# Kernel optimization log

Hardware: AMD Instinct MI355X
Metric: run time of the kernel (lower is better)

Reference implementation:

```python
import jax, jax.numpy as jnp
import numpy as np
import math

D_MODEL = 1024
EPS = 1e-6  # RMSNorm epsilon


def setup_inputs() -> dict:
    key = jax.random.key(0)
    ks = jax.random.split(key, 9)
    d = D_MODEL
    B, T = 4, 4096
    s = 1.0 / math.sqrt(d)
    return {
        "x": jax.random.normal(ks[0], (B, T, d), dtype=jnp.float32),
        "w_key": jax.random.normal(ks[1], (2 * d, d), dtype=jnp.float32) * s,  # Linear(d, 2d, bias=False)
        "conv_w": jax.random.normal(ks[2], (d, 1, 3), dtype=jnp.float32) * (1.0 / math.sqrt(3)),  # depthwise k=3
        "conv_b": jax.random.normal(ks[3], (d,), dtype=jnp.float32) * 0.02,
        "w1": jax.random.normal(ks[4], (2 * d, d), dtype=jnp.float32) * s,  # Linear(d, 2d)
        "b1": jax.random.normal(ks[5], (2 * d,), dtype=jnp.float32) * 0.02,
        "w2": jax.random.normal(ks[6], (d, 2 * d), dtype=jnp.float32) * (1.0 / math.sqrt(2 * d)),  # Linear(2d, d)
        "b2": jax.random.normal(ks[7], (d,), dtype=jnp.float32) * 0.02,
        "norm_w": jnp.ones((d,), dtype=jnp.float32),
    }


def parallel_lerp_scan(theta, alpha):
    # h_t = lerp(h_{t-1}, theta_t, alpha_t) = (1-alpha_t)*h_{t-1} + alpha_t*theta_t
    # Linear recurrence h_t = a_t*h_{t-1} + b_t -> log-depth associative scan.
    a = 1.0 - alpha
    b = alpha * theta

    def combine(c1, c2):
        a1, b1 = c1
        a2, b2 = c2
        return (a2 * a1, a2 * b1 + b2)

    _, h = jax.lax.associative_scan(combine, (a, b), axis=1)
    return h


def rms_norm(x, w):
    var = jnp.mean(jnp.square(x), axis=-1, keepdims=True)
    return x * jax.lax.rsqrt(var + EPS) * w


def reference(x, w_key, conv_w, conv_b, w1, b1, w2, b2, norm_w):
    d = x.shape[-1]
    res = jnp.einsum('btd,ed->bte', x, w_key)  # [B,T,2D]
    theta, alpha = res[..., :d], res[..., d:]
    h = parallel_lerp_scan(jnp.tanh(theta) * math.pi, jax.nn.sigmoid(alpha))
    h = h.astype(x.dtype)
    # causal depthwise conv: left-pad (k-1)=2 zeros along time
    h_t = jnp.transpose(h, (0, 2, 1))  # [B,D,T]
    conv = jax.lax.conv_general_dilated(
        h_t, conv_w, window_strides=(1,), padding=[(2, 0)],
        feature_group_count=d, dimension_numbers=('NCH', 'OIH', 'NCH'))
    h_bound = jnp.transpose(conv + conv_b[None, :, None], (0, 2, 1))  # [B,T,D]
    z = h + h_bound
    hid = jax.nn.silu(jnp.einsum('btd,ed->bte', z, w1) + b1)
    h_final = jnp.einsum('bte,de->btd', hid, w2) + b2
    return rms_norm(h_final, norm_w)
```

## Files before the change

kernel.cpp:

```cpp
#include <hip/hip_runtime.h>

typedef unsigned short u16;
typedef unsigned int u32;
typedef __attribute__((ext_vector_type(8))) short short8;
typedef __attribute__((ext_vector_type(4))) float f32x4;

#define T_LEN 4096
#define BATCH 4
#define M_TOT (BATCH*T_LEN)
#define NCHUNK 32
#define CLEN 128

__device__ __forceinline__ u16 f2bf(float f){
  u32 u = __builtin_bit_cast(u32, f);
  u32 r = (u + 0x7FFFu + ((u >> 16) & 1u)) >> 16;
  return (u16)r;
}
__device__ __forceinline__ float sigmoid_(float v){ return 1.f/(1.f + __expf(-v)); }
__device__ __forceinline__ float tanh_pi_(float v){
  return 3.14159265358979323846f * (1.f - 2.f/(1.f + __expf(2.f*v)));
}

__global__ __launch_bounds__(256) void cvt_bf16_k(const float* __restrict__ in,
                                                  u16* __restrict__ out, int n4){
  int g = blockIdx.x*256 + threadIdx.x;
  if (g >= n4) return;
  float4 v = reinterpret_cast<const float4*>(in)[g];
  reinterpret_cast<ushort4*>(out)[g] =
      make_ushort4(f2bf(v.x), f2bf(v.y), f2bf(v.z), f2bf(v.w));
}


#define BAR() __builtin_amdgcn_s_barrier()
#define WAITLGKM0() asm volatile("s_waitcnt lgkmcnt(0)" ::: "memory")
#define VMCNT(n) asm volatile("s_waitcnt vmcnt(" #n ")" ::: "memory")

#define STAGE(buf, ab, q, kt) do { \
  const u16* _s = ((ab) ? Bb : Ab) + (size_t)(q)*rowK64 + (size_t)(kt)*64; \
  __builtin_amdgcn_global_load_lds( \
    (const __attribute__((address_space(1))) void*)_s, \
    (__attribute__((address_space(3))) void*)(smem + (buf)*65536 + (ab)*32768 + (q)*8192 + stb), \
    16, 0, 0); \
} while(0)

#define LDA(buf, m, kk) (*(const short8*)(smem + (buf)*65536 + aRow + (m)*2048 + ((kk) ? csw1 : csw0)))
#define LDB(buf, n, kk) (*(const short8*)(smem + (buf)*65536 + 32768 + bRow + (n)*2048 + ((kk) ? csw1 : csw0)))

#define LOADB(buf) do { _Pragma("unroll") for (int n=0;n<4;n++){ \
    bfr0[n] = LDB(buf,n,0); bfr1[n] = LDB(buf,n,1); } } while(0)

#define PHASE_Q(buf, q, STMTS, ENDSTMT) do { \
  short8 _a00 = LDA(buf, 2*(q)  , 0); \
  short8 _a01 = LDA(buf, 2*(q)  , 1); \
  short8 _a10 = LDA(buf, 2*(q)+1, 0); \
  short8 _a11 = LDA(buf, 2*(q)+1, 1); \
  STMTS \
  BAR(); \
  WAITLGKM0(); \
  __builtin_amdgcn_s_setprio(1); \
  _Pragma("unroll") \
  for (int n=0;n<4;n++){ \
    acc[2*(q)][n]   = __builtin_amdgcn_mfma_f32_16x16x32_bf16(_a00, bfr0[n], acc[2*(q)][n], 0,0,0); \
    acc[2*(q)][n]   = __builtin_amdgcn_mfma_f32_16x16x32_bf16(_a01, bfr1[n], acc[2*(q)][n], 0,0,0); \
    acc[2*(q)+1][n] = __builtin_amdgcn_mfma_f32_16x16x32_bf16(_a10, bfr0[n], acc[2*(q)+1][n], 0,0,0); \
    acc[2*(q)+1][n] = __builtin_amdgcn_mfma_f32_16x16x32_bf16(_a11, bfr1[n], acc[2*(q)+1][n], 0,0,0); \
  } \
  __builtin_amdgcn_s_setprio(0); \
  ENDSTMT \
  BAR(); \
} while(0)

template<int EPI>
__global__ __launch_bounds__(512, 2) void gemm8p(
    const u16* __restrict__ Ag, const u16* __restrict__ Bg,
    const float* __restrict__ bias, void* __restrict__ Cout,
    int M, int N, int K)
{
  extern __shared__ __attribute__((aligned(16))) char smem[];
  const int tid = threadIdx.x;
  const int wid = tid >> 6, lane = tid & 63;
  const int wr = wid >> 2, wc = wid & 3;
  const int fr = lane & 15, fq = lane >> 4;

  const int nbn = N >> 8;
  const int nwg = gridDim.x;
  const int bid = blockIdx.x;
  const int swzb = (bid & 7) * (nwg >> 3) + (bid >> 3);
  const int bm = swzb / nbn, bn = swzb - bm * nbn;

  const size_t rowK64 = (size_t)64 * K;
  const u16* Ab = Ag + ((size_t)bm*256 + (tid>>3)) * K + ((tid & 7) ^ ((tid >> 3) & 7)) * 8;
  const u16* Bb = Bg + ((size_t)bn*256 + (tid>>3)) * K + ((tid & 7) ^ ((tid >> 3) & 7)) * 8;
  const u32 stb = (u32)(wid << 10);

  const u32 aRow = (u32)(wr*128 + fr) * 128;
  const u32 bRow = (u32)(wc*64  + fr) * 128;
  const u32 csw0 = (u32)((fq*16)      ^ ((fr & 7) << 4));
  const u32 csw1 = (u32)((64 + fq*16) ^ ((fr & 7) << 4));

  f32x4 acc[8][4];
#pragma unroll
  for (int m=0;m<8;m++)
#pragma unroll
    for (int n=0;n<4;n++) acc[m][n] = f32x4{0.f,0.f,0.f,0.f};

  short8 bfr0[4], bfr1[4];

  const int NT = K >> 6;

  STAGE(0,1,0,0); STAGE(0,1,1,0); STAGE(0,1,2,0); STAGE(0,1,3,0);
  STAGE(0,0,0,0); STAGE(0,0,1,0); STAGE(0,0,2,0); STAGE(0,0,3,0);
  STAGE(1,1,0,1); STAGE(1,1,1,1); STAGE(1,1,2,1); STAGE(1,1,3,1);
  STAGE(1,0,0,1); STAGE(1,0,2,1);
  VMCNT(6);
  BAR();

  for (int i = 0; i < (NT>>1) - 1; ++i){
    const int tt = 2*i;
    PHASE_Q(0, 0, LOADB(0); STAGE(1,0,1,tt+1); STAGE(1,0,3,tt+1);, );
    PHASE_Q(0, 1, STAGE(0,1,0,tt+2); STAGE(0,1,1,tt+2);, );
    PHASE_Q(0, 2, STAGE(0,1,2,tt+2); STAGE(0,1,3,tt+2);, );
    PHASE_Q(0, 3, STAGE(0,0,0,tt+2); STAGE(0,0,2,tt+2);, VMCNT(6); );
    PHASE_Q(1, 0, LOADB(1); STAGE(0,0,1,tt+2); STAGE(0,0,3,tt+2);, );
    PHASE_Q(1, 1, STAGE(1,1,0,tt+3); STAGE(1,1,1,tt+3);, );
    PHASE_Q(1, 2, STAGE(1,1,2,tt+3); STAGE(1,1,3,tt+3);, );
    PHASE_Q(1, 3, STAGE(1,0,0,tt+3); STAGE(1,0,2,tt+3);, VMCNT(6); );
  }
  {
    const int tt = NT-2;
    PHASE_Q(0, 0, LOADB(0); STAGE(1,0,1,tt+1); STAGE(1,0,3,tt+1);, );
    PHASE_Q(0, 1, , );
    PHASE_Q(0, 2, , );
    PHASE_Q(0, 3, , VMCNT(0); );
    PHASE_Q(1, 0, LOADB(1);, );
    PHASE_Q(1, 1, , );
    PHASE_Q(1, 2, , );
    PHASE_Q(1, 3, , );
  }

  const int orow0 = bm*256 + wr*128;
  const int ocol0 = bn*256 + wc*64;
#pragma unroll
  for (int m=0;m<8;m++){
#pragma unroll
    for (int n=0;n<4;n++){
      const int col = ocol0 + n*16 + fr;
#pragma unroll
      for (int r=0;r<4;r++){
        const int row = orow0 + m*16 + fq*4 + r;
        float v = acc[m][n][r];
        if constexpr (EPI == 0){
          float o = (col < 1024) ? tanh_pi_(v) : sigmoid_(v);
          ((float*)Cout)[(size_t)row*N + col] = o;
        } else if constexpr (EPI == 1){
          v += bias[col];
          ((u16*)Cout)[(size_t)row*N + col] = f2bf(v * sigmoid_(v));
        } else {
          v += bias[col];
          ((float*)Cout)[(size_t)row*N + col] = v;
        }
      }
    }
  }
}

__global__ __launch_bounds__(256) void scan_stage1(const float* __restrict__ res,
                                                   float* __restrict__ sA,
                                                   float* __restrict__ sB,
                                                   float* __restrict__ sA2,
                                                   float* __restrict__ sB2){
  const int c     = (blockIdx.x & 3)*256 + threadIdx.x;
  const int chunk = (blockIdx.x >> 2) & (NCHUNK-1);
  const int b     = blockIdx.x >> 7;
  const float* p = res + ((size_t)(b*T_LEN + chunk*CLEN))*2048 + c;
  float A = 1.f, Bv = 0.f;
#pragma unroll 4
  for (int t=0;t<CLEN-1;++t){
    float th = p[0];
    float s  = p[1024];
    float a  = 1.f - s;
    A  *= a;
    Bv  = a*Bv + s*th;
    p  += 2048;
  }
  const int idx = (b*NCHUNK + chunk)*1024 + c;
  sA2[idx] = A; sB2[idx] = Bv;
  {
    float th = p[0];
    float s  = p[1024];
    float a  = 1.f - s;
    A  *= a;
    Bv  = a*Bv + s*th;
  }
  sA[idx] = A; sB[idx] = Bv;
}

__global__ __launch_bounds__(256) void scan_stage2(const float* __restrict__ sA,
                                                   const float* __restrict__ sB,
                                                   float* __restrict__ Hp){
  const int g = blockIdx.x*256 + threadIdx.x;
  const int b = g >> 10, c = g & 1023;
  float H = 0.f;
#pragma unroll
  for (int i=0;i<NCHUNK;++i){
    const int idx = (b*NCHUNK + i)*1024 + c;
    Hp[idx] = H;
    H = sA[idx]*H + sB[idx];
  }
}

__global__ __launch_bounds__(256) void scan3_conv_k(const float* __restrict__ res,
                                                    const float* __restrict__ Hp,
                                                    const float* __restrict__ sA2,
                                                    const float* __restrict__ sB2,
                                                    const float* __restrict__ cw,
                                                    const float* __restrict__ cb,
                                                    u16* __restrict__ z){
  const int c     = (blockIdx.x & 3)*256 + threadIdx.x;
  const int chunk = (blockIdx.x >> 2) & (NCHUNK-1);
  const int b     = blockIdx.x >> 7;
  const float* p = res + ((size_t)(b*T_LEN + chunk*CLEN))*2048 + c;
  u16*         q = z   + ((size_t)(b*T_LEN + chunk*CLEN))*1024 + c;
  const int idx = (b*NCHUNK + chunk)*1024 + c;
  float H   = Hp[idx];
  float hm1 = H;
  float hm2 = 0.f;
  if (chunk > 0){
    const int pidx = idx - 1024;
    hm2 = sA2[pidx]*Hp[pidx] + sB2[pidx];
  }
  const float w0 = cw[3*c], w1 = cw[3*c+1], w2 = cw[3*c+2], bb = cb[c];
#pragma unroll 4
  for (int t=0;t<CLEN;++t){
    float th = p[0];
    float s  = p[1024];
    H = (1.f - s)*H + s*th;
    float v = H + bb + hm2*w0 + hm1*w1 + H*w2;
    q[0] = f2bf(v);
    hm2 = hm1; hm1 = H;
    p += 2048; q += 1024;
  }
}

__global__ __launch_bounds__(256) void rmsnorm_k(float* __restrict__ io,
                                                 const float* __restrict__ w){
  const int row = blockIdx.x;
  const int tid = threadIdx.x;
  float* p = io + (size_t)row*1024;
  float4 v = reinterpret_cast<const float4*>(p)[tid];
  float ss = v.x*v.x + v.y*v.y + v.z*v.z + v.w*v.w;
#pragma unroll
  for (int o=32; o>0; o>>=1) ss += __shfl_xor(ss, o, 64);
  __shared__ float red[4];
  if ((tid & 63) == 0) red[tid >> 6] = ss;
  __syncthreads();
  float tot = red[0] + red[1] + red[2] + red[3];
  float scale = rsqrtf(tot * (1.f/1024.f) + 1e-6f);
  float4 wv = reinterpret_cast<const float4*>(w)[tid];
  float4 o;
  o.x = v.x*scale*wv.x; o.y = v.y*scale*wv.y;
  o.z = v.z*scale*wv.z; o.w = v.w*scale*wv.w;
  reinterpret_cast<float4*>(p)[tid] = o;
}

extern "C" void kernel_launch(void* const* d_in, const int* in_sizes, int n_in,
                              void* d_out, int out_size, void* d_ws, size_t ws_size,
                              hipStream_t stream) {
  const float* x      = (const float*)d_in[0];
  const float* w_key  = (const float*)d_in[1];
  const float* conv_w = (const float*)d_in[2];
  const float* conv_b = (const float*)d_in[3];
  const float* w1     = (const float*)d_in[4];
  const float* b1     = (const float*)d_in[5];
  const float* w2     = (const float*)d_in[6];
  const float* b2     = (const float*)d_in[7];
  const float* norm_w = (const float*)d_in[8];
  float* out = (float*)d_out;
  char*  ws  = (char*)d_ws;

  size_t off = 0;
  float* RES  = (float*)(ws + off); off += (size_t)M_TOT*2048*4;
  u16*   XB   = (u16*)  (ws + off); off += (size_t)M_TOT*1024*2;
  u16*   WK   = (u16*)  (ws + off); off += (size_t)2048*1024*2;
  u16*   W1B  = (u16*)  (ws + off); off += (size_t)2048*1024*2;
  u16*   W2B  = (u16*)  (ws + off); off += (size_t)1024*2048*2;
  float* SA   = (float*)(ws + off); off += (size_t)BATCH*NCHUNK*1024*4;
  float* SB   = (float*)(ws + off); off += (size_t)BATCH*NCHUNK*1024*4;
  float* SA2  = (float*)(ws + off); off += (size_t)BATCH*NCHUNK*1024*4;
  float* SB2  = (float*)(ws + off); off += (size_t)BATCH*NCHUNK*1024*4;
  float* HP   = (float*)(ws + off); off += (size_t)BATCH*NCHUNK*1024*4;
  u16* ZB  = XB;
  u16* HID = (u16*)RES;

  hipFuncSetAttribute((const void*)gemm8p<0>, hipFuncAttributeMaxDynamicSharedMemorySize, 131072);
  hipFuncSetAttribute((const void*)gemm8p<1>, hipFuncAttributeMaxDynamicSharedMemorySize, 131072);
  hipFuncSetAttribute((const void*)gemm8p<2>, hipFuncAttributeMaxDynamicSharedMemorySize, 131072);

  cvt_bf16_k<<<(M_TOT*1024/4 + 255)/256, 256, 0, stream>>>(x,     XB,  M_TOT*1024/4);
  cvt_bf16_k<<<(2048*1024/4  + 255)/256, 256, 0, stream>>>(w_key, WK,  2048*1024/4);
  cvt_bf16_k<<<(2048*1024/4  + 255)/256, 256, 0, stream>>>(w1,    W1B, 2048*1024/4);
  cvt_bf16_k<<<(1024*2048/4  + 255)/256, 256, 0, stream>>>(w2,    W2B, 1024*2048/4);

  gemm8p<0><<<(M_TOT/256)*(2048/256), 512, 131072, stream>>>(XB, WK, nullptr, RES, M_TOT, 2048, 1024);

  scan_stage1<<<BATCH*NCHUNK*4, 256, 0, stream>>>(RES, SA, SB, SA2, SB2);
  scan_stage2<<<16, 256, 0, stream>>>(SA, SB, HP);
  scan3_conv_k<<<BATCH*NCHUNK*4, 256, 0, stream>>>(RES, HP, SA2, SB2, conv_w, conv_b, ZB);

  gemm8p<1><<<(M_TOT/256)*(2048/256), 512, 131072, stream>>>(ZB, W1B, b1, HID, M_TOT, 2048, 1024);

  gemm8p<2><<<(M_TOT/256)*(1024/256), 512, 131072, stream>>>(HID, W2B, b2, out, M_TOT, 1024, 2048);

  rmsnorm_k<<<M_TOT, 256, 0, stream>>>(out, norm_w);
}
```

Before: 328.8 us.

## Software-pipeline LDS fragment loads in GEMM and store scan input as bf16

The GEMM main loop now double-buffers A and B register fragments, issuing the LDS reads for the next quarter-phase during the current MFMA block so LDS latency is hidden behind compute. Separately, the first GEMM's activated theta/alpha output is written as bf16 instead of fp32, halving traffic for that write and for the two scan kernels that read it. The register double-buffering raises VGPR pressure, which could cause spills under the two-blocks-per-CU launch bound. Storing scan inputs in bf16 also reduces the precision of the recurrence inputs.

```diff
diff --git a/kernel.cpp b/kernel.cpp
--- a/kernel.cpp
+++ b/kernel.cpp
@@ -15,6 +15,9 @@
   u32 u = __builtin_bit_cast(u32, f);
   u32 r = (u + 0x7FFFu + ((u >> 16) & 1u)) >> 16;
   return (u16)r;
+}
+__device__ __forceinline__ float bf2f(u16 h){
+  u32 u = ((u32)h) << 16; return __builtin_bit_cast(float, u);
 }
 __device__ __forceinline__ float sigmoid_(float v){ return 1.f/(1.f + __expf(-v)); }
 __device__ __forceinline__ float tanh_pi_(float v){
@@ -30,7 +33,6 @@
       make_ushort4(f2bf(v.x), f2bf(v.y), f2bf(v.z), f2bf(v.w));
 }
 
-
 #define BAR() __builtin_amdgcn_s_barrier()
 #define WAITLGKM0() asm volatile("s_waitcnt lgkmcnt(0)" ::: "memory")
 #define VMCNT(n) asm volatile("s_waitcnt vmcnt(" #n ")" ::: "memory")
@@ -46,29 +48,25 @@
 #define LDA(buf, m, kk) (*(const short8*)(smem + (buf)*65536 + aRow + (m)*2048 + ((kk) ? csw1 : csw0)))
 #define LDB(buf, n, kk) (*(const short8*)(smem + (buf)*65536 + 32768 + bRow + (n)*2048 + ((kk) ? csw1 : csw0)))
 
-#define LOADB(buf) do { _Pragma("unroll") for (int n=0;n<4;n++){ \
-    bfr0[n] = LDB(buf,n,0); bfr1[n] = LDB(buf,n,1); } } while(0)
-
-#define PHASE_Q(buf, q, STMTS, ENDSTMT) do { \
-  short8 _a00 = LDA(buf, 2*(q)  , 0); \
-  short8 _a01 = LDA(buf, 2*(q)  , 1); \
-  short8 _a10 = LDA(buf, 2*(q)+1, 0); \
-  short8 _a11 = LDA(buf, 2*(q)+1, 1); \
-  STMTS \
-  BAR(); \
-  WAITLGKM0(); \
-  __builtin_amdgcn_s_setprio(1); \
-  _Pragma("unroll") \
+#define PFA(dst, buf, q) do { \
+  dst[0] = LDA(buf, 2*(q),   0); \
+  dst[1] = LDA(buf, 2*(q),   1); \
+  dst[2] = LDA(buf, 2*(q)+1, 0); \
+  dst[3] = LDA(buf, 2*(q)+1, 1); } while(0)
+
+#define PFB(d0, d1, buf) do { _Pragma("unroll") \
+  for (int n=0;n<4;n++){ d0[n] = LDB(buf,n,0); d1[n] = LDB(buf,n,1); } } while(0)
+
+#define MFMA_Q(q, A, B0, B1) do { _Pragma("unroll") \
   for (int n=0;n<4;n++){ \
-    acc[2*(q)][n]   = __builtin_amdgcn_mfma_f32_16x16x32_bf16(_a00, bfr0[n], acc[2*(q)][n], 0,0,0); \
-    acc[2*(q)][n]   = __builtin_amdgcn_mfma_f32_16x16x32_bf16(_a01, bfr1[n], acc[2*(q)][n], 0,0,0); \
-    acc[2*(q)+1][n] = __builtin_amdgcn_mfma_f32_16x16x32_bf16(_a10, bfr0[n], acc[2*(q)+1][n], 0,0,0); \
-    acc[2*(q)+1][n] = __builtin_amdgcn_mfma_f32_16x16x32_bf16(_a11, bfr1[n], acc[2*(q)+1][n], 0,0,0); \
-  } \
-  __builtin_amdgcn_s_setprio(0); \
-  ENDSTMT \
-  BAR(); \
-} while(0)
+    acc[2*(q)][n]   = __builtin_amdgcn_mfma_f32_16x16x32_bf16(A[0], B0[n], acc[2*(q)][n], 0,0,0); \
+    acc[2*(q)][n]   = __builtin_amdgcn_mfma_f32_16x16x32_bf16(A[1], B1[n], acc[2*(q)][n], 0,0,0); \
+    acc[2*(q)+1][n] = __builtin_amdgcn_mfma_f32_16x16x32_bf16(A[2], B0[n], acc[2*(q)+1][n], 0,0,0); \
+    acc[2*(q)+1][n] = __builtin_amdgcn_mfma_f32_16x16x32_bf16(A[3], B1[n], acc[2*(q)+1][n], 0,0,0); \
+  } } while(0)
+
+#define PRIO1() __builtin_amdgcn_s_setprio(1)
+#define PRIO0() __builtin_amdgcn_s_setprio(0)
 
 template<int EPI>
 __global__ __launch_bounds__(512, 2) void gemm8p(
@@ -104,7 +102,8 @@
 #pragma unroll
     for (int n=0;n<4;n++) acc[m][n] = f32x4{0.f,0.f,0.f,0.f};
 
-  short8 bfr0[4], bfr1[4];
+  short8 bP0[4], bP1[4], bN0[4], bN1[4];
+  short8 aP[4], aN[4];
 
   const int NT = K >> 6;
 
@@ -114,28 +113,69 @@
   STAGE(1,0,0,1); STAGE(1,0,2,1);
   VMCNT(6);
   BAR();
+  PFB(bP0, bP1, 0);
+  PFA(aP, 0, 0);
 
   for (int i = 0; i < (NT>>1) - 1; ++i){
     const int tt = 2*i;
-    PHASE_Q(0, 0, LOADB(0); STAGE(1,0,1,tt+1); STAGE(1,0,3,tt+1);, );
-    PHASE_Q(0, 1, STAGE(0,1,0,tt+2); STAGE(0,1,1,tt+2);, );
-    PHASE_Q(0, 2, STAGE(0,1,2,tt+2); STAGE(0,1,3,tt+2);, );
-    PHASE_Q(0, 3, STAGE(0,0,0,tt+2); STAGE(0,0,2,tt+2);, VMCNT(6); );
-    PHASE_Q(1, 0, LOADB(1); STAGE(0,0,1,tt+2); STAGE(0,0,3,tt+2);, );
-    PHASE_Q(1, 1, STAGE(1,1,0,tt+3); STAGE(1,1,1,tt+3);, );
-    PHASE_Q(1, 2, STAGE(1,1,2,tt+3); STAGE(1,1,3,tt+3);, );
-    PHASE_Q(1, 3, STAGE(1,0,0,tt+3); STAGE(1,0,2,tt+3);, VMCNT(6); );
+    STAGE(1,0,1,tt+1); STAGE(1,0,3,tt+1);
+    BAR(); WAITLGKM0();
+    PRIO1(); MFMA_Q(0, aP, bP0, bP1); PFA(aN, 0, 1); PRIO0();
+    BAR();
+    STAGE(0,1,0,tt+2); STAGE(0,1,1,tt+2);
+    BAR(); WAITLGKM0();
+    PRIO1(); MFMA_Q(1, aN, bP0, bP1); PFA(aP, 0, 2); PRIO0();
+    BAR();
+    STAGE(0,1,2,tt+2); STAGE(0,1,3,tt+2);
+    BAR(); WAITLGKM0();
+    PRIO1(); MFMA_Q(2, aP, bP0, bP1); PFA(aN, 0, 3); PRIO0();
+    BAR();
+    STAGE(0,0,0,tt+2); STAGE(0,0,2,tt+2);
+    BAR(); WAITLGKM0(); VMCNT(6);
+    PRIO1(); MFMA_Q(3, aN, bP0, bP1); PFB(bN0, bN1, 1); PFA(aP, 1, 0); PRIO0();
+    BAR();
+    STAGE(0,0,1,tt+2); STAGE(0,0,3,tt+2);
+    BAR(); WAITLGKM0();
+    PRIO1(); MFMA_Q(0, aP, bN0, bN1); PFA(aN, 1, 1); PRIO0();
+    BAR();
+    STAGE(1,1,0,tt+3); STAGE(1,1,1,tt+3);
+    BAR(); WAITLGKM0();
+    PRIO1(); MFMA_Q(1, aN, bN0, bN1); PFA(aP, 1, 2); PRIO0();
+    BAR();
+    STAGE(1,1,2,tt+3); STAGE(1,1,3,tt+3);
+    BAR(); WAITLGKM0();
+    PRIO1(); MFMA_Q(2, aP, bN0, bN1); PFA(aN, 1, 3); PRIO0();
+    BAR();
+    STAGE(1,0,0,tt+3); STAGE(1,0,2,tt+3);
+    BAR(); WAITLGKM0(); VMCNT(6);
+    PRIO1(); MFMA_Q(3, aN, bN0, bN1); PFB(bP0, bP1, 0); PFA(aP, 0, 0); PRIO0();
+    BAR();
   }
   {
-    const int tt = NT-2;
-    PHASE_Q(0, 0, LOADB(0); STAGE(1,0,1,tt+1); STAGE(1,0,3,tt+1);, );
-    PHASE_Q(0, 1, , );
-    PHASE_Q(0, 2, , );
-    PHASE_Q(0, 3, , VMCNT(0); );
-    PHASE_Q(1, 0, LOADB(1);, );
-    PHASE_Q(1, 1, , );
-    PHASE_Q(1, 2, , );
-    PHASE_Q(1, 3, , );
+    STAGE(1,0,1,NT-1); STAGE(1,0,3,NT-1);
+    BAR(); WAITLGKM0();
+    PRIO1(); MFMA_Q(0, aP, bP0, bP1); PFA(aN, 0, 1); PRIO0();
+    BAR();
+    BAR(); WAITLGKM0();
+    PRIO1(); MFMA_Q(1, aN, bP0, bP1); PFA(aP, 0, 2); PRIO0();
+    BAR();
+    BAR(); WAITLGKM0();
+    PRIO1(); MFMA_Q(2, aP, bP0, bP1); PFA(aN, 0, 3); PRIO0();
+    BAR();
+    BAR(); WAITLGKM0(); VMCNT(0);
+    PRIO1(); MFMA_Q(3, aN, bP0, bP1); PFB(bN0, bN1, 1); PFA(aP, 1, 0); PRIO0();
+    BAR();
+    BAR(); WAITLGKM0();
+    PRIO1(); MFMA_Q(0, aP, bN0, bN1); PFA(aN, 1, 1); PRIO0();
+    BAR();
+    BAR(); WAITLGKM0();
+    PRIO1(); MFMA_Q(1, aN, bN0, bN1); PFA(aP, 1, 2); PRIO0();
+    BAR();
+    BAR(); WAITLGKM0();
+    PRIO1(); MFMA_Q(2, aP, bN0, bN1); PFA(aN, 1, 3); PRIO0();
+    BAR();
+    BAR(); WAITLGKM0();
+    PRIO1(); MFMA_Q(3, aN, bN0, bN1); PRIO0();
   }
 
   const int orow0 = bm*256 + wr*128;
@@ -151,7 +191,7 @@
         float v = acc[m][n][r];
         if constexpr (EPI == 0){
           float o = (col < 1024) ? tanh_pi_(v) : sigmoid_(v);
-          ((float*)Cout)[(size_t)row*N + col] = o;
+          ((u16*)Cout)[(size_t)row*N + col] = f2bf(o);
         } else if constexpr (EPI == 1){
           v += bias[col];
           ((u16*)Cout)[(size_t)row*N + col] = f2bf(v * sigmoid_(v));
@@ -164,7 +204,7 @@
   }
 }
 
-__global__ __launch_bounds__(256) void scan_stage1(const float* __restrict__ res,
+__global__ __launch_bounds__(256) void scan_stage1(const u16* __restrict__ res,
                                                    float* __restrict__ sA,
                                                    float* __restrict__ sB,
                                                    float* __restrict__ sA2,
@@ -172,12 +212,12 @@
   const int c     = (blockIdx.x & 3)*256 + threadIdx.x;
   const int chunk = (blockIdx.x >> 2) & (NCHUNK-1);
   const int b     = blockIdx.x >> 7;
-  const float* p = res + ((size_t)(b*T_LEN + chunk*CLEN))*2048 + c;
+  const u16* p = res + ((size_t)(b*T_LEN + chunk*CLEN))*2048 + c;
   float A = 1.f, Bv = 0.f;
 #pragma unroll 4
   for (int t=0;t<CLEN-1;++t){
-    float th = p[0];
-    float s  = p[1024];
+    float th = bf2f(p[0]);
+    float s  = bf2f(p[1024]);
     float a  = 1.f - s;
     A  *= a;
     Bv  = a*Bv + s*th;
@@ -186,8 +226,8 @@
   const int idx = (b*NCHUNK + chunk)*1024 + c;
   sA2[idx] = A; sB2[idx] = Bv;
   {
-    float th = p[0];
-    float s  = p[1024];
+    float th = bf2f(p[0]);
+    float s  = bf2f(p[1024]);
     float a  = 1.f - s;
     A  *= a;
     Bv  = a*Bv + s*th;
@@ -209,7 +249,7 @@
   }
 }
 
-__global__ __launch_bounds__(256) void scan3_conv_k(const float* __restrict__ res,
+__global__ __launch_bounds__(256) void scan3_conv_k(const u16* __restrict__ res,
                                                     const float* __restrict__ Hp,
                                                     const float* __restrict__ sA2,
                                                     const float* __restrict__ sB2,
@@ -219,8 +259,8 @@
   const int c     = (blockIdx.x & 3)*256 + threadIdx.x;
   const int chunk = (blockIdx.x >> 2) & (NCHUNK-1);
   const int b     = blockIdx.x >> 7;
-  const float* p = res + ((size_t)(b*T_LEN + chunk*CLEN))*2048 + c;
-  u16*         q = z   + ((size_t)(b*T_LEN + chunk*CLEN))*1024 + c;
+  const u16* p = res + ((size_t)(b*T_LEN + chunk*CLEN))*2048 + c;
+  u16*       q = z   + ((size_t)(b*T_LEN + chunk*CLEN))*1024 + c;
   const int idx = (b*NCHUNK + chunk)*1024 + c;
   float H   = Hp[idx];
   float hm1 = H;
@@ -232,8 +272,8 @@
   const float w0 = cw[3*c], w1 = cw[3*c+1], w2 = cw[3*c+2], bb = cb[c];
 #pragma unroll 4
   for (int t=0;t<CLEN;++t){
-    float th = p[0];
-    float s  = p[1024];
+    float th = bf2f(p[0]);
+    float s  = bf2f(p[1024]);
     H = (1.f - s)*H + s*th;
     float v = H + bb + hm2*w0 + hm1*w1 + H*w2;
     q[0] = f2bf(v);
@@ -279,7 +319,7 @@
   char*  ws  = (char*)d_ws;
 
   size_t off = 0;
-  float* RES  = (float*)(ws + off); off += (size_t)M_TOT*2048*4;
+  u16*   RES  = (u16*)  (ws + off); off += (size_t)M_TOT*2048*2;
   u16*   XB   = (u16*)  (ws + off); off += (size_t)M_TOT*1024*2;
   u16*   WK   = (u16*)  (ws + off); off += (size_t)2048*1024*2;
   u16*   W1B  = (u16*)  (ws + off); off += (size_t)2048*1024*2;
@@ -290,7 +330,7 @@
   float* SB2  = (float*)(ws + off); off += (size_t)BATCH*NCHUNK*1024*4;
   float* HP   = (float*)(ws + off); off += (size_t)BATCH*NCHUNK*1024*4;
   u16* ZB  = XB;
-  u16* HID = (u16*)RES;
+  u16* HID = RES;
 
   hipFuncSetAttribute((const void*)gemm8p<0>, hipFuncAttributeMaxDynamicSharedMemorySize, 131072);
   hipFuncSetAttribute((const void*)gemm8p<1>, hipFuncAttributeMaxDynamicSharedMemorySize, 131072);
```

After: 316.8 us. 3.6% less time.
